# Kernel tuning notes

Hardware: AMD Instinct MI355X
Metric: run time of the kernel (lower is better)

Reference implementation:

```python
import jax, jax.numpy as jnp
import numpy as np

B, T, NIN, NMEM, NOUT = 8, 2048, 1024, 1024, 1024


def setup_inputs() -> dict:
    key = jax.random.key(0)
    ks = jax.random.split(key, 9)
    s_in = 1.0 / np.sqrt(NIN).astype(np.float32)
    s_mem = 1.0 / np.sqrt(NMEM).astype(np.float32)
    return {
        "x": jax.random.normal(ks[0], (B, T, NIN), jnp.float32),
        "mem": jnp.zeros((B, NMEM), jnp.float32),
        # torch Linear weights are [out_features, in_features]
        "wr_w": jax.random.normal(ks[1], (NMEM, NIN), jnp.float32) * s_in,
        "wr_b": jax.random.normal(ks[2], (NMEM,), jnp.float32) * s_in,
        "wi_w": jax.random.normal(ks[3], (NMEM, NIN), jnp.float32) * s_in,
        "wig_w": jax.random.normal(ks[4], (NMEM, NIN), jnp.float32) * s_in,
        "wig_b": jax.random.normal(ks[5], (NMEM,), jnp.float32) * s_in,
        "wog_w": jax.random.normal(ks[6], (NMEM, NIN), jnp.float32) * s_in,
        "wog_b": jax.random.normal(ks[7], (NMEM,), jnp.float32) * s_in,
        "wo_w": jax.random.normal(ks[8], (NOUT, NMEM), jnp.float32) * s_mem,
    }


def _sqrll_scan(xi, r, mem0):
    # linear recurrence: h_t = h_{t-1} * r_t + x_t, over time axis
    def step(h, inp):
        xt, rt = inp
        h = h * rt + xt
        return h, h

    # time-major for scan: [T, B, M]
    _, ys = jax.lax.scan(step, mem0, (jnp.swapaxes(xi, 0, 1), jnp.swapaxes(r, 0, 1)))
    return jnp.swapaxes(ys, 0, 1)  # [B, T, M]


def reference(x, mem, wr_w, wr_b, wi_w, wig_w, wig_b, wog_w, wog_b, wo_w):
    og = jax.nn.sigmoid(jnp.einsum("bti,mi->btm", x, wog_w) + wog_b)
    r = jax.nn.sigmoid(jnp.einsum("bti,mi->btm", x, wr_w) + wr_b)
    xi = jnp.einsum("bti,mi->btm", x, wi_w) * jax.nn.sigmoid(
        jnp.einsum("bti,mi->btm", x, wig_w) + wig_b
    )
    y = _sqrll_scan(xi, r, mem)  # [B, T, NMEM]
    mem_out = jax.lax.stop_gradient(y[:, -1])
    y = jax.nn.soft_sign(y) * og
    y = jnp.einsum("btm,om->bto", y, wo_w)
    return (y, mem_out)
```

## Files before the change

kernel.cpp:

```cpp
#include <hip/hip_runtime.h>
#include <hip/hip_bf16.h>
#include <cstdint>
#include <cstddef>

using bf16 = __hip_bfloat16;

typedef short s16x8 __attribute__((ext_vector_type(8)));
typedef short s16x4 __attribute__((ext_vector_type(4)));
typedef float f32x4 __attribute__((ext_vector_type(4)));

#define CH 32
#define CS 64

__device__ __align__(16) bf16  g_xb[16384 * 1024];
__device__ __align__(16) bf16  g_wb[5 * 1024 * 1024];
__device__ __align__(16) bf16  g_og[16384 * 1024];
__device__ float g_cA[CH * 8192];
__device__ float g_cB[CH * 8192];

__device__ inline short bfbits(float f) {
  unsigned x = __float_as_uint(f);
  return (short)((x + 0x7FFFu + ((x >> 16) & 1u)) >> 16);
}
__device__ inline float sigmoidf_(float z) { return 1.0f / (1.0f + __expf(-z)); }

__device__ inline void gload_lds16(const void* g, void* l) {
  __builtin_amdgcn_global_load_lds(
      (const __attribute__((address_space(1))) void*)g,
      (__attribute__((address_space(3))) void*)l, 16, 0, 0);
}

__global__ void conv_kernel(const float* __restrict__ src, bf16* __restrict__ dst, int n4) {
  int i = blockIdx.x * blockDim.x + threadIdx.x;
  const int stride = gridDim.x * blockDim.x;
  for (; i < n4; i += stride) {
    f32x4 v = ((const f32x4*)src)[i];
    s16x4 w;
    w[0] = bfbits(v[0]); w[1] = bfbits(v[1]);
    w[2] = bfbits(v[2]); w[3] = bfbits(v[3]);
    ((s16x4*)dst)[i] = w;
  }
}

__global__ __launch_bounds__(512, 2) void gemm_quad(
    const bf16* __restrict__ A,
    const bf16* __restrict__ B0, const bf16* __restrict__ B1,
    const bf16* __restrict__ B2, const bf16* __restrict__ B3,
    const float* __restrict__ bias_r, const float* __restrict__ bias_og,
    const float* __restrict__ bias_ig,
    float* __restrict__ Cr, bf16* __restrict__ Cog, bf16* __restrict__ Cxi,
    int M, int N, int K)
{
  __shared__ bf16 As[2][256 * 64];
  __shared__ bf16 Bs[2][4][64 * 64];

  const int tid  = threadIdx.x;
  const int wave = tid >> 6;
  const int lane = tid & 63;
  const int m0 = blockIdx.x * 256;
  const int n0 = blockIdx.y * 64;

  const int srow8 = lane >> 3;
  const int schk8 = ((lane & 7) ^ ((lane >> 3) & 7)) << 3;
  const bf16* Bm = (wave < 2) ? B0 : (wave < 4) ? B1 : (wave < 6) ? B2 : B3;
  const bf16* pAs = A  + (size_t)(m0 + wave * 32 + srow8) * K + schk8;
  const bf16* pBs = Bm + (size_t)(n0 + (wave & 1) * 32 + srow8) * K + schk8;

  const int lane15 = lane & 15;
  const int csel   = lane >> 4;
  int o[2];
  #pragma unroll
  for (int kk = 0; kk < 2; ++kk)
    o[kk] = lane15 * 64 + ((((kk << 2) + csel) ^ (lane15 & 7)) << 3);
  const int wmA = (wave & 3) * 4096;
  const int mlo = (wave >> 2) * 2;

  f32x4 accP[4][4] = {};
  f32x4 accQ[4][4] = {};

  auto stage = [&](int b, size_t koff) {
    #pragma unroll
    for (int q = 0; q < 4; ++q) {
      gload_lds16(pAs + (size_t)q * 8 * K + koff,
                  (void*)&As[b][wave * 2048 + q * 512]);
      gload_lds16(pBs + (size_t)q * 8 * K + koff,
                  (void*)&Bs[b][wave >> 1][(wave & 1) * 2048 + q * 512]);
    }
  };

  int buf = 0;
  stage(0, 0);
  asm volatile("s_waitcnt vmcnt(0)" ::: "memory");
  __builtin_amdgcn_s_barrier();
  __builtin_amdgcn_sched_barrier(0);

  for (int t = 0; t < 16; ++t) {
    if (t + 1 < 16) stage(buf ^ 1, (size_t)(t + 1) * 64);
    __builtin_amdgcn_sched_barrier(0);

    #pragma unroll
    for (int kk = 0; kk < 2; ++kk) {
      const bf16* aB  = &As[buf][wmA + o[kk]];
      const bf16* b0B = &Bs[buf][mlo][o[kk]];
      const bf16* b1B = &Bs[buf][mlo + 1][o[kk]];
      s16x8 af[4], f0[4], f1[4];
      #pragma unroll
      for (int i = 0; i < 4; ++i) af[i] = *(const s16x8*)(aB + i * 1024);
      #pragma unroll
      for (int j = 0; j < 4; ++j) {
        f0[j] = *(const s16x8*)(b0B + j * 1024);
        f1[j] = *(const s16x8*)(b1B + j * 1024);
      }
      __builtin_amdgcn_s_setprio(1);
      #pragma unroll
      for (int i = 0; i < 4; ++i)
        #pragma unroll
        for (int j = 0; j < 4; ++j) {
          accP[i][j] = __builtin_amdgcn_mfma_f32_16x16x32_bf16(af[i], f0[j], accP[i][j], 0, 0, 0);
          accQ[i][j] = __builtin_amdgcn_mfma_f32_16x16x32_bf16(af[i], f1[j], accQ[i][j], 0, 0, 0);
        }
      __builtin_amdgcn_s_setprio(0);
    }

    asm volatile("s_waitcnt vmcnt(0)" ::: "memory");
    __builtin_amdgcn_s_barrier();
    __builtin_amdgcn_sched_barrier(0);
    buf ^= 1;
  }

  const int rq = (lane >> 4) * 4;
  const int cl = lane & 15;
  const int wr0 = m0 + (wave & 3) * 64;
  if (wave < 4) {
    #pragma unroll
    for (int j = 0; j < 4; ++j) {
      const int gc = n0 + j * 16 + cl;
      const float bR = bias_r[gc];
      const float bO = bias_og[gc];
      #pragma unroll
      for (int i = 0; i < 4; ++i) {
        const int gr = wr0 + i * 16 + rq;
        #pragma unroll
        for (int rr = 0; rr < 4; ++rr) {
          const size_t idx = (size_t)(gr + rr) * N + gc;
          Cr[idx]  = sigmoidf_(accP[i][j][rr] + bR);
          Cog[idx] = __float2bfloat16(sigmoidf_(accQ[i][j][rr] + bO));
        }
      }
    }
  } else {
    #pragma unroll
    for (int j = 0; j < 4; ++j) {
      const int gc = n0 + j * 16 + cl;
      const float bG = bias_ig[gc];
      #pragma unroll
      for (int i = 0; i < 4; ++i) {
        const int gr = wr0 + i * 16 + rq;
        #pragma unroll
        for (int rr = 0; rr < 4; ++rr) {
          const size_t idx = (size_t)(gr + rr) * N + gc;
          Cxi[idx] = __float2bfloat16(accP[i][j][rr] * sigmoidf_(accQ[i][j][rr] + bG));
        }
      }
    }
  }
}

__global__ __launch_bounds__(512, 2) void gemm_single(
    const bf16* __restrict__ A, const bf16* __restrict__ Bw,
    float* __restrict__ C, int M, int N, int K)
{
  __shared__ bf16 As[3][256 * 64];
  __shared__ bf16 Bs[3][128 * 64];

  const int tid  = threadIdx.x;
  const int wave = tid >> 6;
  const int lane = tid & 63;
  const int m0 = blockIdx.x * 256;
  const int n0 = blockIdx.y * 128;
  const int wm = (wave >> 1) * 64;
  const int wn = (wave & 1) * 64;

  const int srow8 = lane >> 3;
  const int schk8 = ((lane & 7) ^ ((lane >> 3) & 7)) << 3;
  const bf16* pAs = A  + (size_t)(m0 + wave * 32 + srow8) * K + schk8;
  const bf16* pBs = Bw + (size_t)(n0 + wave * 16 + srow8) * K + schk8;

  const int lane15 = lane & 15;
  const int csel   = lane >> 4;
  int o[2];
  #pragma unroll
  for (int kk = 0; kk < 2; ++kk)
    o[kk] = lane15 * 64 + ((((kk << 2) + csel) ^ (lane15 & 7)) << 3);

  f32x4 acc[4][4] = {};

  auto stage = [&](int b, size_t koff) {
    #pragma unroll
    for (int q = 0; q < 4; ++q)
      gload_lds16(pAs + (size_t)q * 8 * K + koff,
                  (void*)&As[b][wave * 2048 + q * 512]);
    #pragma unroll
    for (int q = 0; q < 2; ++q)
      gload_lds16(pBs + (size_t)q * 8 * K + koff,
                  (void*)&Bs[b][wave * 1024 + q * 512]);
  };

  stage(0, 0);
  stage(1, 64);
  asm volatile("s_waitcnt vmcnt(6)" ::: "memory");
  __builtin_amdgcn_s_barrier();
  __builtin_amdgcn_sched_barrier(0);

  int cur = 0, nxt = 2;
  for (int t = 0; t < 16; ++t) {
    const bool pf = (t + 2 < 16);
    if (pf) stage(nxt, (size_t)(t + 2) * 64);
    __builtin_amdgcn_sched_barrier(0);

    #pragma unroll
    for (int kk = 0; kk < 2; ++kk) {
      const bf16* aB = &As[cur][wm * 64 + o[kk]];
      const bf16* bB = &Bs[cur][wn * 64 + o[kk]];
      s16x8 af[4], bfr[4];
      #pragma unroll
      for (int i = 0; i < 4; ++i) af[i] = *(const s16x8*)(aB + i * 1024);
      #pragma unroll
      for (int j = 0; j < 4; ++j) bfr[j] = *(const s16x8*)(bB + j * 1024);
      __builtin_amdgcn_s_setprio(1);
      #pragma unroll
      for (int i = 0; i < 4; ++i)
        #pragma unroll
        for (int j = 0; j < 4; ++j)
          acc[i][j] = __builtin_amdgcn_mfma_f32_16x16x32_bf16(af[i], bfr[j], acc[i][j], 0, 0, 0);
      __builtin_amdgcn_s_setprio(0);
    }

    if (pf) asm volatile("s_waitcnt vmcnt(6)" ::: "memory");
    else    asm volatile("s_waitcnt vmcnt(0)" ::: "memory");
    __builtin_amdgcn_s_barrier();
    __builtin_amdgcn_sched_barrier(0);

    cur = (cur + 1 == 3) ? 0 : cur + 1;
    nxt = (nxt + 1 == 3) ? 0 : nxt + 1;
  }

  const int rq = (lane >> 4) * 4;
  const int cl = lane & 15;
  #pragma unroll
  for (int j = 0; j < 4; ++j) {
    const int gc = n0 + wn + j * 16 + cl;
    #pragma unroll
    for (int i = 0; i < 4; ++i) {
      const int gr = m0 + wm + i * 16 + rq;
      #pragma unroll
      for (int rr = 0; rr < 4; ++rr)
        C[(size_t)(gr + rr) * N + gc] = acc[i][j][rr];
    }
  }
}

__global__ __launch_bounds__(256) void scan_p1(
    const float* __restrict__ r, const bf16* __restrict__ xi)
{
  const int bid = blockIdx.x;
  const int c   = bid >> 5;
  const int idx = (bid & 31) * 256 + threadIdx.x;
  const int b = idx >> 10, m = idx & 1023;
  const size_t base = ((size_t)b * 2048 + c * CS) * 1024 + m;
  float a = 1.0f, s = 0.0f;
  #pragma unroll 16
  for (int t = 0; t < CS; ++t) {
    const size_t o = base + (size_t)t * 1024;
    const float rv = r[o];
    const float xv = __bfloat162float(xi[o]);
    a *= rv;
    s = fmaf(s, rv, xv);
  }
  g_cA[c * 8192 + idx] = a;
  g_cB[c * 8192 + idx] = s;
}

__global__ __launch_bounds__(256) void scan_p2(
    const float* __restrict__ mem, float* __restrict__ memout)
{
  const int idx = blockIdx.x * 256 + threadIdx.x;
  float H = mem[idx];
  #pragma unroll
  for (int c = 0; c < CH; ++c) {
    const float a = g_cA[c * 8192 + idx];
    const float s = g_cB[c * 8192 + idx];
    g_cA[c * 8192 + idx] = H;
    H = fmaf(a, H, s);
  }
  memout[idx] = H;
}

__global__ __launch_bounds__(256) void scan_p3(
    const float* __restrict__ r, bf16* xi, const bf16* __restrict__ og)
{
  const int bid = blockIdx.x;
  const int c   = bid >> 5;
  const int idx = (bid & 31) * 256 + threadIdx.x;
  const int b = idx >> 10, m = idx & 1023;
  const size_t base = ((size_t)b * 2048 + c * CS) * 1024 + m;
  float h = g_cA[c * 8192 + idx];
  #pragma unroll 8
  for (int t = 0; t < CS; ++t) {
    const size_t o = base + (size_t)t * 1024;
    const float rv = r[o];
    const float xv = __bfloat162float(xi[o]);
    const float ov = __bfloat162float(og[o]);
    h = fmaf(h, rv, xv);
    xi[o] = __float2bfloat16(h / (1.0f + fabsf(h)) * ov);
  }
}

extern "C" void kernel_launch(void* const* d_in, const int* in_sizes, int n_in,
                              void* d_out, int out_size, void* d_ws, size_t ws_size,
                              hipStream_t stream)
{
  const float* x     = (const float*)d_in[0];
  const float* mem   = (const float*)d_in[1];
  const float* wr_w  = (const float*)d_in[2];
  const float* wr_b  = (const float*)d_in[3];
  const float* wi_w  = (const float*)d_in[4];
  const float* wig_w = (const float*)d_in[5];
  const float* wig_b = (const float*)d_in[6];
  const float* wog_w = (const float*)d_in[7];
  const float* wog_b = (const float*)d_in[8];
  const float* wo_w  = (const float*)d_in[9];
  float* out = (float*)d_out;

  const int M = 16384, N = 1024, K = 1024;
  const size_t MN = (size_t)M * N;

  float* r  = (float*)d_ws;
  bf16*  xi = (bf16*)((char*)d_ws + MN * 4);

  bf16* xb = nullptr, *wb = nullptr, *og = nullptr;
  hipGetSymbolAddress((void**)&xb, HIP_SYMBOL(g_xb));
  hipGetSymbolAddress((void**)&wb, HIP_SYMBOL(g_wb));
  hipGetSymbolAddress((void**)&og, HIP_SYMBOL(g_og));

  dim3 block(256);

  conv_kernel<<<dim3(2048), block, 0, stream>>>(x, xb, (int)(MN / 4));
  const int W4 = 1024 * 1024 / 4;
  conv_kernel<<<dim3(256), block, 0, stream>>>(wr_w,  wb + 0 * 1024 * 1024, W4);
  conv_kernel<<<dim3(256), block, 0, stream>>>(wi_w,  wb + 1 * 1024 * 1024, W4);
  conv_kernel<<<dim3(256), block, 0, stream>>>(wig_w, wb + 2 * 1024 * 1024, W4);
  conv_kernel<<<dim3(256), block, 0, stream>>>(wog_w, wb + 3 * 1024 * 1024, W4);
  conv_kernel<<<dim3(256), block, 0, stream>>>(wo_w,  wb + 4 * 1024 * 1024, W4);

  gemm_quad<<<dim3(64, 16), dim3(512), 0, stream>>>(
      xb,
      wb + 0 * 1024 * 1024,
      wb + 3 * 1024 * 1024,
      wb + 1 * 1024 * 1024,
      wb + 2 * 1024 * 1024,
      wr_b, wog_b, wig_b,
      r, og, xi, M, N, K);

  scan_p1<<<dim3(1024), block, 0, stream>>>(r, xi);
  scan_p2<<<dim3(32),   block, 0, stream>>>(mem, out + MN);
  scan_p3<<<dim3(1024), block, 0, stream>>>(r, xi, og);

  gemm_single<<<dim3(64, 8), dim3(512), 0, stream>>>(
      xi, wb + 4 * 1024 * 1024, out, M, N, K);
}
```

Measured before the change: 453.0 us.

## Deepen GEMM pipelines to 4-stage K=32 buffers and swap grid order

Both GEMM kernels now use K-tiles of 32 instead of 64 with a 4-deep LDS ring buffer. Three stages stay in flight, waited on with vmcnt counts instead of full drains. The grid is transposed so consecutive blocks share the same M rows and walk N, which should improve L2 reuse of the activation tiles. The cost is more barriers per K (32 iterations instead of 16) and fewer MFMAs between each sync.

```diff
diff --git a/kernel.cpp b/kernel.cpp
--- a/kernel.cpp
+++ b/kernel.cpp
@@ -51,82 +51,87 @@
     float* __restrict__ Cr, bf16* __restrict__ Cog, bf16* __restrict__ Cxi,
     int M, int N, int K)
 {
-  __shared__ bf16 As[2][256 * 64];
-  __shared__ bf16 Bs[2][4][64 * 64];
+  __shared__ bf16 As[4][256 * 32];
+  __shared__ bf16 Bs[4][4][64 * 32];
 
   const int tid  = threadIdx.x;
   const int wave = tid >> 6;
   const int lane = tid & 63;
-  const int m0 = blockIdx.x * 256;
-  const int n0 = blockIdx.y * 64;
-
-  const int srow8 = lane >> 3;
-  const int schk8 = ((lane & 7) ^ ((lane >> 3) & 7)) << 3;
+  const int n0 = blockIdx.x * 64;
+  const int m0 = blockIdx.y * 256;
+
+  const int srow16 = lane >> 2;
+  const int schk   = ((lane & 3) ^ ((lane >> 2) & 3)) << 3;
   const bf16* Bm = (wave < 2) ? B0 : (wave < 4) ? B1 : (wave < 6) ? B2 : B3;
-  const bf16* pAs = A  + (size_t)(m0 + wave * 32 + srow8) * K + schk8;
-  const bf16* pBs = Bm + (size_t)(n0 + (wave & 1) * 32 + srow8) * K + schk8;
+  const bf16* pAs = A  + (size_t)(m0 + wave * 32 + srow16) * K + schk;
+  const bf16* pBs = Bm + (size_t)(n0 + (wave & 1) * 32 + srow16) * K + schk;
+  const size_t krow16 = (size_t)16 * K;
 
   const int lane15 = lane & 15;
   const int csel   = lane >> 4;
-  int o[2];
-  #pragma unroll
-  for (int kk = 0; kk < 2; ++kk)
-    o[kk] = lane15 * 64 + ((((kk << 2) + csel) ^ (lane15 & 7)) << 3);
-  const int wmA = (wave & 3) * 4096;
+  const int o = lane15 * 32 + ((csel ^ (lane15 & 3)) << 3);
+  const int wmA = (wave & 3) * 2048;
   const int mlo = (wave >> 2) * 2;
 
   f32x4 accP[4][4] = {};
   f32x4 accQ[4][4] = {};
 
   auto stage = [&](int b, size_t koff) {
-    #pragma unroll
-    for (int q = 0; q < 4; ++q) {
-      gload_lds16(pAs + (size_t)q * 8 * K + koff,
-                  (void*)&As[b][wave * 2048 + q * 512]);
-      gload_lds16(pBs + (size_t)q * 8 * K + koff,
-                  (void*)&Bs[b][wave >> 1][(wave & 1) * 2048 + q * 512]);
+    bf16* as = &As[b][wave * 1024];
+    bf16* bs = &Bs[b][wave >> 1][(wave & 1) * 1024];
+    gload_lds16(pAs + koff,          (void*)as);
+    gload_lds16(pAs + krow16 + koff, (void*)(as + 512));
+    gload_lds16(pBs + koff,          (void*)bs);
+    gload_lds16(pBs + krow16 + koff, (void*)(bs + 512));
+  };
+
+  auto compute = [&](int c) {
+    const bf16* aB  = &As[c][wmA + o];
+    const bf16* b0B = &Bs[c][mlo][o];
+    const bf16* b1B = &Bs[c][mlo + 1][o];
+    s16x8 af[4], f0[4], f1[4];
+    #pragma unroll
+    for (int i = 0; i < 4; ++i) af[i] = *(const s16x8*)(aB + i * 512);
+    #pragma unroll
+    for (int j = 0; j < 4; ++j) {
+      f0[j] = *(const s16x8*)(b0B + j * 512);
+      f1[j] = *(const s16x8*)(b1B + j * 512);
     }
+    __builtin_amdgcn_s_setprio(1);
+    #pragma unroll
+    for (int i = 0; i < 4; ++i)
+      #pragma unroll
+      for (int j = 0; j < 4; ++j) {
+        accP[i][j] = __builtin_amdgcn_mfma_f32_16x16x32_bf16(af[i], f0[j], accP[i][j], 0, 0, 0);
+        accQ[i][j] = __builtin_amdgcn_mfma_f32_16x16x32_bf16(af[i], f1[j], accQ[i][j], 0, 0, 0);
+      }
+    __builtin_amdgcn_s_setprio(0);
   };
 
-  int buf = 0;
   stage(0, 0);
-  asm volatile("s_waitcnt vmcnt(0)" ::: "memory");
-  __builtin_amdgcn_s_barrier();
-  __builtin_amdgcn_sched_barrier(0);
-
-  for (int t = 0; t < 16; ++t) {
-    if (t + 1 < 16) stage(buf ^ 1, (size_t)(t + 1) * 64);
+  stage(1, 32);
+  stage(2, 64);
+  asm volatile("s_waitcnt vmcnt(8)" ::: "memory");
+  __builtin_amdgcn_s_barrier();
+  __builtin_amdgcn_sched_barrier(0);
+
+  for (int t = 0; t < 29; ++t) {
+    stage((t + 3) & 3, (size_t)(t + 3) * 32);
     __builtin_amdgcn_sched_barrier(0);
-
-    #pragma unroll
-    for (int kk = 0; kk < 2; ++kk) {
-      const bf16* aB  = &As[buf][wmA + o[kk]];
-      const bf16* b0B = &Bs[buf][mlo][o[kk]];
-      const bf16* b1B = &Bs[buf][mlo + 1][o[kk]];
-      s16x8 af[4], f0[4], f1[4];
-      #pragma unroll
-      for (int i = 0; i < 4; ++i) af[i] = *(const s16x8*)(aB + i * 1024);
-      #pragma unroll
-      for (int j = 0; j < 4; ++j) {
-        f0[j] = *(const s16x8*)(b0B + j * 1024);
-        f1[j] = *(const s16x8*)(b1B + j * 1024);
-      }
-      __builtin_amdgcn_s_setprio(1);
-      #pragma unroll
-      for (int i = 0; i < 4; ++i)
-        #pragma unroll
-        for (int j = 0; j < 4; ++j) {
-          accP[i][j] = __builtin_amdgcn_mfma_f32_16x16x32_bf16(af[i], f0[j], accP[i][j], 0, 0, 0);
-          accQ[i][j] = __builtin_amdgcn_mfma_f32_16x16x32_bf16(af[i], f1[j], accQ[i][j], 0, 0, 0);
-        }
-      __builtin_amdgcn_s_setprio(0);
-    }
-
-    asm volatile("s_waitcnt vmcnt(0)" ::: "memory");
+    compute(t & 3);
+    asm volatile("s_waitcnt vmcnt(8)" ::: "memory");
     __builtin_amdgcn_s_barrier();
     __builtin_amdgcn_sched_barrier(0);
-    buf ^= 1;
-  }
+  }
+  compute(29 & 3);
+  asm volatile("s_waitcnt vmcnt(4)" ::: "memory");
+  __builtin_amdgcn_s_barrier();
+  __builtin_amdgcn_sched_barrier(0);
+  compute(30 & 3);
+  asm volatile("s_waitcnt vmcnt(0)" ::: "memory");
+  __builtin_amdgcn_s_barrier();
+  __builtin_amdgcn_sched_barrier(0);
+  compute(31 & 3);
 
   const int rq = (lane >> 4) * 4;
   const int cl = lane & 15;
@@ -170,80 +175,77 @@
     const bf16* __restrict__ A, const bf16* __restrict__ Bw,
     float* __restrict__ C, int M, int N, int K)
 {
-  __shared__ bf16 As[3][256 * 64];
-  __shared__ bf16 Bs[3][128 * 64];
+  __shared__ bf16 As[4][256 * 32];
+  __shared__ bf16 Bs[4][128 * 32];
 
   const int tid  = threadIdx.x;
   const int wave = tid >> 6;
   const int lane = tid & 63;
-  const int m0 = blockIdx.x * 256;
-  const int n0 = blockIdx.y * 128;
+  const int n0 = blockIdx.x * 128;
+  const int m0 = blockIdx.y * 256;
   const int wm = (wave >> 1) * 64;
   const int wn = (wave & 1) * 64;
 
-  const int srow8 = lane >> 3;
-  const int schk8 = ((lane & 7) ^ ((lane >> 3) & 7)) << 3;
-  const bf16* pAs = A  + (size_t)(m0 + wave * 32 + srow8) * K + schk8;
-  const bf16* pBs = Bw + (size_t)(n0 + wave * 16 + srow8) * K + schk8;
+  const int srow16 = lane >> 2;
+  const int schk   = ((lane & 3) ^ ((lane >> 2) & 3)) << 3;
+  const bf16* pAs = A  + (size_t)(m0 + wave * 32 + srow16) * K + schk;
+  const bf16* pBs = Bw + (size_t)(n0 + wave * 16 + srow16) * K + schk;
+  const size_t krow16 = (size_t)16 * K;
 
   const int lane15 = lane & 15;
   const int csel   = lane >> 4;
-  int o[2];
-  #pragma unroll
-  for (int kk = 0; kk < 2; ++kk)
-    o[kk] = lane15 * 64 + ((((kk << 2) + csel) ^ (lane15 & 7)) << 3);
+  const int o = lane15 * 32 + ((csel ^ (lane15 & 3)) << 3);
 
   f32x4 acc[4][4] = {};
 
   auto stage = [&](int b, size_t koff) {
-    #pragma unroll
-    for (int q = 0; q < 4; ++q)
-      gload_lds16(pAs + (size_t)q * 8 * K + koff,
-                  (void*)&As[b][wave * 2048 + q * 512]);
-    #pragma unroll
-    for (int q = 0; q < 2; ++q)
-      gload_lds16(pBs + (size_t)q * 8 * K + koff,
-                  (void*)&Bs[b][wave * 1024 + q * 512]);
+    bf16* as = &As[b][wave * 1024];
+    gload_lds16(pAs + koff,          (void*)as);
+    gload_lds16(pAs + krow16 + koff, (void*)(as + 512));
+    gload_lds16(pBs + koff,          (void*)&Bs[b][wave * 512]);
   };
 
+  auto compute = [&](int c) {
+    const bf16* aB = &As[c][wm * 32 + o];
+    const bf16* bB = &Bs[c][wn * 32 + o];
+    s16x8 af[4], bfr[4];
+    #pragma unroll
+    for (int i = 0; i < 4; ++i) af[i] = *(const s16x8*)(aB + i * 512);
+    #pragma unroll
+    for (int j = 0; j < 4; ++j) bfr[j] = *(const s16x8*)(bB + j * 512);
+    __builtin_amdgcn_s_setprio(1);
+    #pragma unroll
+    for (int i = 0; i < 4; ++i)
+      #pragma unroll
+      for (int j = 0; j < 4; ++j)
+        acc[i][j] = __builtin_amdgcn_mfma_f32_16x16x32_bf16(af[i], bfr[j], acc[i][j], 0, 0, 0);
+    __builtin_amdgcn_s_setprio(0);
+  };
+
   stage(0, 0);
-  stage(1, 64);
+  stage(1, 32);
+  stage(2, 64);
   asm volatile("s_waitcnt vmcnt(6)" ::: "memory");
   __builtin_amdgcn_s_barrier();
   __builtin_amdgcn_sched_barrier(0);
 
-  int cur = 0, nxt = 2;
-  for (int t = 0; t < 16; ++t) {
-    const bool pf = (t + 2 < 16);
-    if (pf) stage(nxt, (size_t)(t + 2) * 64);
+  for (int t = 0; t < 29; ++t) {
+    stage((t + 3) & 3, (size_t)(t + 3) * 32);
     __builtin_amdgcn_sched_barrier(0);
-
-    #pragma unroll
-    for (int kk = 0; kk < 2; ++kk) {
-      const bf16* aB = &As[cur][wm * 64 + o[kk]];
-      const bf16* bB = &Bs[cur][wn * 64 + o[kk]];
-      s16x8 af[4], bfr[4];
-      #pragma unroll
-      for (int i = 0; i < 4; ++i) af[i] = *(const s16x8*)(aB + i * 1024);
-      #pragma unroll
-      for (int j = 0; j < 4; ++j) bfr[j] = *(const s16x8*)(bB + j * 1024);
-      __builtin_amdgcn_s_setprio(1);
-      #pragma unroll
-      for (int i = 0; i < 4; ++i)
-        #pragma unroll
-        for (int j = 0; j < 4; ++j)
-          acc[i][j] = __builtin_amdgcn_mfma_f32_16x16x32_bf16(af[i], bfr[j], acc[i][j], 0, 0, 0);
-      __builtin_amdgcn_s_setprio(0);
-    }
-
-    if (pf) asm volatile("s_waitcnt vmcnt(6)" ::: "memory");
-    else    asm volatile("s_waitcnt vmcnt(0)" ::: "memory");
+    compute(t & 3);
+    asm volatile("s_waitcnt vmcnt(6)" ::: "memory");
     __builtin_amdgcn_s_barrier();
     __builtin_amdgcn_sched_barrier(0);
-
-    cur = (cur + 1 == 3) ? 0 : cur + 1;
-    nxt = (nxt + 1 == 3) ? 0 : nxt + 1;
-  }
+  }
+  compute(29 & 3);
+  asm volatile("s_waitcnt vmcnt(3)" ::: "memory");
+  __builtin_amdgcn_s_barrier();
+  __builtin_amdgcn_sched_barrier(0);
+  compute(30 & 3);
+  asm volatile("s_waitcnt vmcnt(0)" ::: "memory");
+  __builtin_amdgcn_s_barrier();
+  __builtin_amdgcn_sched_barrier(0);
+  compute(31 & 3);
 
   const int rq = (lane >> 4) * 4;
   const int cl = lane & 15;
@@ -353,7 +355,7 @@
   conv_kernel<<<dim3(256), block, 0, stream>>>(wog_w, wb + 3 * 1024 * 1024, W4);
   conv_kernel<<<dim3(256), block, 0, stream>>>(wo_w,  wb + 4 * 1024 * 1024, W4);
 
-  gemm_quad<<<dim3(64, 16), dim3(512), 0, stream>>>(
+  gemm_quad<<<dim3(16, 64), dim3(512), 0, stream>>>(
       xb,
       wb + 0 * 1024 * 1024,
       wb + 3 * 1024 * 1024,
@@ -366,6 +368,6 @@
   scan_p2<<<dim3(32),   block, 0, stream>>>(mem, out + MN);
   scan_p3<<<dim3(1024), block, 0, stream>>>(r, xi, og);
 
-  gemm_single<<<dim3(64, 8), dim3(512), 0, stream>>>(
+  gemm_single<<<dim3(8, 64), dim3(512), 0, stream>>>(
       xi, wb + 4 * 1024 * 1024, out, M, N, K);
 }
```

New measurement: 509.8 us. +12.5%, slower.

## Load GEMM weight fragments directly into registers, bypassing LDS staging

Applied to the files above, without the earlier changes.

Both GEMM kernels stop staging the B (weight) tile through shared memory. Each wave now loads its MFMA B fragments straight from global memory into registers, double-buffered across k-steps, while A keeps a triple-buffered LDS pipeline. The warp tiling changes to 128 rows by 16 or 32 columns per wave, and the quad kernel now fuses all three epilogues in each wave. The aim is to cut LDS traffic and footprint and to overlap weight loads with compute, at the cost of uncoalesced global B loads and more register pressure.

```diff
diff --git a/kernel.cpp b/kernel.cpp
--- a/kernel.cpp
+++ b/kernel.cpp
@@ -51,117 +51,119 @@
     float* __restrict__ Cr, bf16* __restrict__ Cog, bf16* __restrict__ Cxi,
     int M, int N, int K)
 {
-  __shared__ bf16 As[2][256 * 64];
-  __shared__ bf16 Bs[2][4][64 * 64];
+  __shared__ bf16 As[3][256 * 64];
 
   const int tid  = threadIdx.x;
   const int wave = tid >> 6;
   const int lane = tid & 63;
   const int m0 = blockIdx.x * 256;
   const int n0 = blockIdx.y * 64;
+  const int mrow = wave >> 2;
+  const int ncol = wave & 3;
 
   const int srow8 = lane >> 3;
-  const int schk8 = ((lane & 7) ^ ((lane >> 3) & 7)) << 3;
-  const bf16* Bm = (wave < 2) ? B0 : (wave < 4) ? B1 : (wave < 6) ? B2 : B3;
-  const bf16* pAs = A  + (size_t)(m0 + wave * 32 + srow8) * K + schk8;
-  const bf16* pBs = Bm + (size_t)(n0 + (wave & 1) * 32 + srow8) * K + schk8;
+  const int schk  = ((lane & 7) ^ ((lane >> 3) & 7)) << 3;
+  const bf16* pAs = A + (size_t)(m0 + wave * 32 + srow8) * K + schk;
 
   const int lane15 = lane & 15;
   const int csel   = lane >> 4;
-  int o[2];
+  int oA[2];
   #pragma unroll
   for (int kk = 0; kk < 2; ++kk)
-    o[kk] = lane15 * 64 + ((((kk << 2) + csel) ^ (lane15 & 7)) << 3);
-  const int wmA = (wave & 3) * 4096;
-  const int mlo = (wave >> 2) * 2;
-
-  f32x4 accP[4][4] = {};
-  f32x4 accQ[4][4] = {};
-
-  auto stage = [&](int b, size_t koff) {
-    #pragma unroll
-    for (int q = 0; q < 4; ++q) {
-      gload_lds16(pAs + (size_t)q * 8 * K + koff,
-                  (void*)&As[b][wave * 2048 + q * 512]);
-      gload_lds16(pBs + (size_t)q * 8 * K + koff,
-                  (void*)&Bs[b][wave >> 1][(wave & 1) * 2048 + q * 512]);
-    }
-  };
-
-  int buf = 0;
-  stage(0, 0);
-  asm volatile("s_waitcnt vmcnt(0)" ::: "memory");
-  __builtin_amdgcn_s_barrier();
-  __builtin_amdgcn_sched_barrier(0);
-
-  for (int t = 0; t < 16; ++t) {
-    if (t + 1 < 16) stage(buf ^ 1, (size_t)(t + 1) * 64);
-    __builtin_amdgcn_sched_barrier(0);
-
+    oA[kk] = lane15 * 64 + ((((kk << 2) + csel) ^ (lane15 & 7)) << 3);
+
+  const size_t bOffL = (size_t)(n0 + ncol * 16 + lane15) * K + csel * 8;
+
+  f32x4 acc[4][8] = {};
+
+  auto stageA = [&](int b, int t) {
+    const size_t koff = (size_t)t * 64;
+    bf16* dst = &As[b][wave * 2048];
+    gload_lds16(pAs + koff,                   (void*)dst);
+    gload_lds16(pAs + koff + (size_t)8  * K,  (void*)(dst + 512));
+    gload_lds16(pAs + koff + (size_t)16 * K,  (void*)(dst + 1024));
+    gload_lds16(pAs + koff + (size_t)24 * K,  (void*)(dst + 1536));
+  };
+
+  auto loadB = [&](s16x8 (&d)[4][2], int t) {
+    const size_t kb = bOffL + (size_t)t * 64;
+    d[0][0] = *(const s16x8*)(B0 + kb); d[0][1] = *(const s16x8*)(B0 + kb + 32);
+    d[1][0] = *(const s16x8*)(B1 + kb); d[1][1] = *(const s16x8*)(B1 + kb + 32);
+    d[2][0] = *(const s16x8*)(B2 + kb); d[2][1] = *(const s16x8*)(B2 + kb + 32);
+    d[3][0] = *(const s16x8*)(B3 + kb); d[3][1] = *(const s16x8*)(B3 + kb + 32);
+  };
+
+  auto compute = [&](int t, const s16x8 (&bq)[4][2]) {
+    const bf16* Ab = &As[t % 3][mrow * 8192];
     #pragma unroll
     for (int kk = 0; kk < 2; ++kk) {
-      const bf16* aB  = &As[buf][wmA + o[kk]];
-      const bf16* b0B = &Bs[buf][mlo][o[kk]];
-      const bf16* b1B = &Bs[buf][mlo + 1][o[kk]];
-      s16x8 af[4], f0[4], f1[4];
-      #pragma unroll
-      for (int i = 0; i < 4; ++i) af[i] = *(const s16x8*)(aB + i * 1024);
-      #pragma unroll
-      for (int j = 0; j < 4; ++j) {
-        f0[j] = *(const s16x8*)(b0B + j * 1024);
-        f1[j] = *(const s16x8*)(b1B + j * 1024);
+      s16x8 af[8];
+      const int ob = oA[kk];
+      #pragma unroll
+      for (int i = 0; i < 8; ++i) af[i] = *(const s16x8*)(Ab + ob + i * 1024);
+      __builtin_amdgcn_s_setprio(1);
+      #pragma unroll
+      for (int i = 0; i < 8; ++i) {
+        acc[0][i] = __builtin_amdgcn_mfma_f32_16x16x32_bf16(af[i], bq[0][kk], acc[0][i], 0, 0, 0);
+        acc[1][i] = __builtin_amdgcn_mfma_f32_16x16x32_bf16(af[i], bq[1][kk], acc[1][i], 0, 0, 0);
+        acc[2][i] = __builtin_amdgcn_mfma_f32_16x16x32_bf16(af[i], bq[2][kk], acc[2][i], 0, 0, 0);
+        acc[3][i] = __builtin_amdgcn_mfma_f32_16x16x32_bf16(af[i], bq[3][kk], acc[3][i], 0, 0, 0);
       }
-      __builtin_amdgcn_s_setprio(1);
-      #pragma unroll
-      for (int i = 0; i < 4; ++i)
-        #pragma unroll
-        for (int j = 0; j < 4; ++j) {
-          accP[i][j] = __builtin_amdgcn_mfma_f32_16x16x32_bf16(af[i], f0[j], accP[i][j], 0, 0, 0);
-          accQ[i][j] = __builtin_amdgcn_mfma_f32_16x16x32_bf16(af[i], f1[j], accQ[i][j], 0, 0, 0);
-        }
       __builtin_amdgcn_s_setprio(0);
     }
-
-    asm volatile("s_waitcnt vmcnt(0)" ::: "memory");
+  };
+
+  s16x8 bEven[4][2], bOdd[4][2];
+
+  stageA(0, 0);
+  stageA(1, 1);
+  loadB(bEven, 0);
+  asm volatile("s_waitcnt vmcnt(12)" ::: "memory");
+  __builtin_amdgcn_s_barrier();
+  __builtin_amdgcn_sched_barrier(0);
+
+  #pragma unroll 1
+  for (int d = 0; d < 7; ++d) {
+    const int t = 2 * d;
+    stageA((t + 2) % 3, t + 2);
+    loadB(bOdd, t + 1);
+    __builtin_amdgcn_sched_barrier(0);
+    compute(t, bEven);
+    asm volatile("s_waitcnt vmcnt(12)" ::: "memory");
     __builtin_amdgcn_s_barrier();
     __builtin_amdgcn_sched_barrier(0);
-    buf ^= 1;
-  }
+
+    stageA((t + 3) % 3, t + 3);
+    loadB(bEven, t + 2);
+    __builtin_amdgcn_sched_barrier(0);
+    compute(t + 1, bOdd);
+    asm volatile("s_waitcnt vmcnt(12)" ::: "memory");
+    __builtin_amdgcn_s_barrier();
+    __builtin_amdgcn_sched_barrier(0);
+  }
+  loadB(bOdd, 15);
+  __builtin_amdgcn_sched_barrier(0);
+  compute(14, bEven);
+  asm volatile("s_waitcnt vmcnt(8)" ::: "memory");
+  __builtin_amdgcn_s_barrier();
+  __builtin_amdgcn_sched_barrier(0);
+  compute(15, bOdd);
 
   const int rq = (lane >> 4) * 4;
   const int cl = lane & 15;
-  const int wr0 = m0 + (wave & 3) * 64;
-  if (wave < 4) {
+  const int gc = n0 + ncol * 16 + cl;
+  const float bR = bias_r[gc];
+  const float bO = bias_og[gc];
+  const float bG = bias_ig[gc];
+  #pragma unroll
+  for (int i = 0; i < 8; ++i) {
+    const int gr = m0 + mrow * 128 + i * 16 + rq;
     #pragma unroll
-    for (int j = 0; j < 4; ++j) {
-      const int gc = n0 + j * 16 + cl;
-      const float bR = bias_r[gc];
-      const float bO = bias_og[gc];
-      #pragma unroll
-      for (int i = 0; i < 4; ++i) {
-        const int gr = wr0 + i * 16 + rq;
-        #pragma unroll
-        for (int rr = 0; rr < 4; ++rr) {
-          const size_t idx = (size_t)(gr + rr) * N + gc;
-          Cr[idx]  = sigmoidf_(accP[i][j][rr] + bR);
-          Cog[idx] = __float2bfloat16(sigmoidf_(accQ[i][j][rr] + bO));
-        }
-      }
-    }
-  } else {
-    #pragma unroll
-    for (int j = 0; j < 4; ++j) {
-      const int gc = n0 + j * 16 + cl;
-      const float bG = bias_ig[gc];
-      #pragma unroll
-      for (int i = 0; i < 4; ++i) {
-        const int gr = wr0 + i * 16 + rq;
-        #pragma unroll
-        for (int rr = 0; rr < 4; ++rr) {
-          const size_t idx = (size_t)(gr + rr) * N + gc;
-          Cxi[idx] = __float2bfloat16(accP[i][j][rr] * sigmoidf_(accQ[i][j][rr] + bG));
-        }
-      }
+    for (int rr = 0; rr < 4; ++rr) {
+      const size_t idx = (size_t)(gr + rr) * N + gc;
+      Cr[idx]  = sigmoidf_(acc[0][i][rr] + bR);
+      Cog[idx] = __float2bfloat16(sigmoidf_(acc[1][i][rr] + bO));
+      Cxi[idx] = __float2bfloat16(acc[2][i][rr] * sigmoidf_(acc[3][i][rr] + bG));
     }
   }
 }
@@ -171,91 +173,111 @@
     float* __restrict__ C, int M, int N, int K)
 {
   __shared__ bf16 As[3][256 * 64];
-  __shared__ bf16 Bs[3][128 * 64];
 
   const int tid  = threadIdx.x;
   const int wave = tid >> 6;
   const int lane = tid & 63;
   const int m0 = blockIdx.x * 256;
   const int n0 = blockIdx.y * 128;
-  const int wm = (wave >> 1) * 64;
-  const int wn = (wave & 1) * 64;
+  const int mrow = wave >> 2;
+  const int ncol = wave & 3;
 
   const int srow8 = lane >> 3;
-  const int schk8 = ((lane & 7) ^ ((lane >> 3) & 7)) << 3;
-  const bf16* pAs = A  + (size_t)(m0 + wave * 32 + srow8) * K + schk8;
-  const bf16* pBs = Bw + (size_t)(n0 + wave * 16 + srow8) * K + schk8;
+  const int schk  = ((lane & 7) ^ ((lane >> 3) & 7)) << 3;
+  const bf16* pAs = A + (size_t)(m0 + wave * 32 + srow8) * K + schk;
 
   const int lane15 = lane & 15;
   const int csel   = lane >> 4;
-  int o[2];
+  int oA[2];
   #pragma unroll
   for (int kk = 0; kk < 2; ++kk)
-    o[kk] = lane15 * 64 + ((((kk << 2) + csel) ^ (lane15 & 7)) << 3);
-
-  f32x4 acc[4][4] = {};
-
-  auto stage = [&](int b, size_t koff) {
-    #pragma unroll
-    for (int q = 0; q < 4; ++q)
-      gload_lds16(pAs + (size_t)q * 8 * K + koff,
-                  (void*)&As[b][wave * 2048 + q * 512]);
-    #pragma unroll
-    for (int q = 0; q < 2; ++q)
-      gload_lds16(pBs + (size_t)q * 8 * K + koff,
-                  (void*)&Bs[b][wave * 1024 + q * 512]);
-  };
-
-  stage(0, 0);
-  stage(1, 64);
-  asm volatile("s_waitcnt vmcnt(6)" ::: "memory");
-  __builtin_amdgcn_s_barrier();
-  __builtin_amdgcn_sched_barrier(0);
-
-  int cur = 0, nxt = 2;
-  for (int t = 0; t < 16; ++t) {
-    const bool pf = (t + 2 < 16);
-    if (pf) stage(nxt, (size_t)(t + 2) * 64);
-    __builtin_amdgcn_sched_barrier(0);
-
+    oA[kk] = lane15 * 64 + ((((kk << 2) + csel) ^ (lane15 & 7)) << 3);
+
+  const size_t bOff0 = (size_t)(n0 + ncol * 32 + lane15) * K + csel * 8;
+  const size_t bOff1 = bOff0 + (size_t)16 * K;
+
+  f32x4 acc[2][8] = {};
+
+  auto stageA = [&](int b, int t) {
+    const size_t koff = (size_t)t * 64;
+    bf16* dst = &As[b][wave * 2048];
+    gload_lds16(pAs + koff,                  (void*)dst);
+    gload_lds16(pAs + koff + (size_t)8  * K, (void*)(dst + 512));
+    gload_lds16(pAs + koff + (size_t)16 * K, (void*)(dst + 1024));
+    gload_lds16(pAs + koff + (size_t)24 * K, (void*)(dst + 1536));
+  };
+
+  auto loadB = [&](s16x8 (&d)[2][2], int t) {
+    const size_t kb = (size_t)t * 64;
+    d[0][0] = *(const s16x8*)(Bw + bOff0 + kb); d[0][1] = *(const s16x8*)(Bw + bOff0 + kb + 32);
+    d[1][0] = *(const s16x8*)(Bw + bOff1 + kb); d[1][1] = *(const s16x8*)(Bw + bOff1 + kb + 32);
+  };
+
+  auto compute = [&](int t, const s16x8 (&bq)[2][2]) {
+    const bf16* Ab = &As[t % 3][mrow * 8192];
     #pragma unroll
     for (int kk = 0; kk < 2; ++kk) {
-      const bf16* aB = &As[cur][wm * 64 + o[kk]];
-      const bf16* bB = &Bs[cur][wn * 64 + o[kk]];
-      s16x8 af[4], bfr[4];
-      #pragma unroll
-      for (int i = 0; i < 4; ++i) af[i] = *(const s16x8*)(aB + i * 1024);
-      #pragma unroll
-      for (int j = 0; j < 4; ++j) bfr[j] = *(const s16x8*)(bB + j * 1024);
+      s16x8 af[8];
+      const int ob = oA[kk];
+      #pragma unroll
+      for (int i = 0; i < 8; ++i) af[i] = *(const s16x8*)(Ab + ob + i * 1024);
       __builtin_amdgcn_s_setprio(1);
       #pragma unroll
-      for (int i = 0; i < 4; ++i)
-        #pragma unroll
-        for (int j = 0; j < 4; ++j)
-          acc[i][j] = __builtin_amdgcn_mfma_f32_16x16x32_bf16(af[i], bfr[j], acc[i][j], 0, 0, 0);
+      for (int i = 0; i < 8; ++i) {
+        acc[0][i] = __builtin_amdgcn_mfma_f32_16x16x32_bf16(af[i], bq[0][kk], acc[0][i], 0, 0, 0);
+        acc[1][i] = __builtin_amdgcn_mfma_f32_16x16x32_bf16(af[i], bq[1][kk], acc[1][i], 0, 0, 0);
+      }
       __builtin_amdgcn_s_setprio(0);
     }
-
-    if (pf) asm volatile("s_waitcnt vmcnt(6)" ::: "memory");
-    else    asm volatile("s_waitcnt vmcnt(0)" ::: "memory");
+  };
+
+  s16x8 bEven[2][2], bOdd[2][2];
+
+  stageA(0, 0);
+  stageA(1, 1);
+  loadB(bEven, 0);
+  asm volatile("s_waitcnt vmcnt(8)" ::: "memory");
+  __builtin_amdgcn_s_barrier();
+  __builtin_amdgcn_sched_barrier(0);
+
+  #pragma unroll 1
+  for (int d = 0; d < 7; ++d) {
+    const int t = 2 * d;
+    stageA((t + 2) % 3, t + 2);
+    loadB(bOdd, t + 1);
+    __builtin_amdgcn_sched_barrier(0);
+    compute(t, bEven);
+    asm volatile("s_waitcnt vmcnt(8)" ::: "memory");
     __builtin_amdgcn_s_barrier();
     __builtin_amdgcn_sched_barrier(0);
 
-    cur = (cur + 1 == 3) ? 0 : cur + 1;
-    nxt = (nxt + 1 == 3) ? 0 : nxt + 1;
-  }
+    stageA((t + 3) % 3, t + 3);
+    loadB(bEven, t + 2);
+    __builtin_amdgcn_sched_barrier(0);
+    compute(t + 1, bOdd);
+    asm volatile("s_waitcnt vmcnt(8)" ::: "memory");
+    __builtin_amdgcn_s_barrier();
+    __builtin_amdgcn_sched_barrier(0);
+  }
+  loadB(bOdd, 15);
+  __builtin_amdgcn_sched_barrier(0);
+  compute(14, bEven);
+  asm volatile("s_waitcnt vmcnt(4)" ::: "memory");
+  __builtin_amdgcn_s_barrier();
+  __builtin_amdgcn_sched_barrier(0);
+  compute(15, bOdd);
 
   const int rq = (lane >> 4) * 4;
   const int cl = lane & 15;
   #pragma unroll
-  for (int j = 0; j < 4; ++j) {
-    const int gc = n0 + wn + j * 16 + cl;
+  for (int j = 0; j < 2; ++j) {
+    const int gc = n0 + ncol * 32 + j * 16 + cl;
     #pragma unroll
-    for (int i = 0; i < 4; ++i) {
-      const int gr = m0 + wm + i * 16 + rq;
+    for (int i = 0; i < 8; ++i) {
+      const int gr = m0 + mrow * 128 + i * 16 + rq;
       #pragma unroll
       for (int rr = 0; rr < 4; ++rr)
-        C[(size_t)(gr + rr) * N + gc] = acc[i][j][rr];
+        C[(size_t)(gr + rr) * N + gc] = acc[j][i][rr];
     }
   }
 }
```

New measurement: 492.1 us. 8.6% more time.

## Shrink GEMM tiles to 128 rows, BK=32, triple-buffered 256-thread blocks

Applied to the files above, without the earlier changes.

Both GEMMs switch from 512-thread blocks with 256-row tiles and a 64-wide K step to 256-thread blocks with 128-row tiles and a 32-wide K step. Each uses a unified LDS buffer with a new 4-chunk XOR swizzle and a three-stage global_load_lds pipeline. The intent is more blocks for better CU fill and occupancy, plus deeper prefetch to hide load latency. In exchange, each block reuses less data, so more global and L2 traffic is needed, and there are twice as many barriers per K pass.

```diff
diff --git a/kernel.cpp b/kernel.cpp
--- a/kernel.cpp
+++ b/kernel.cpp
@@ -42,7 +42,7 @@
   }
 }
 
-__global__ __launch_bounds__(512, 2) void gemm_quad(
+__global__ __launch_bounds__(256, 2) void gemm_quad(
     const bf16* __restrict__ A,
     const bf16* __restrict__ B0, const bf16* __restrict__ B1,
     const bf16* __restrict__ B2, const bf16* __restrict__ B3,
@@ -51,87 +51,95 @@
     float* __restrict__ Cr, bf16* __restrict__ Cog, bf16* __restrict__ Cxi,
     int M, int N, int K)
 {
-  __shared__ bf16 As[2][256 * 64];
-  __shared__ bf16 Bs[2][4][64 * 64];
+  __shared__ bf16 Ls[3][12288];
 
   const int tid  = threadIdx.x;
   const int wave = tid >> 6;
   const int lane = tid & 63;
-  const int m0 = blockIdx.x * 256;
+  const int m0 = blockIdx.x * 128;
   const int n0 = blockIdx.y * 64;
-
-  const int srow8 = lane >> 3;
-  const int schk8 = ((lane & 7) ^ ((lane >> 3) & 7)) << 3;
-  const bf16* Bm = (wave < 2) ? B0 : (wave < 4) ? B1 : (wave < 6) ? B2 : B3;
-  const bf16* pAs = A  + (size_t)(m0 + wave * 32 + srow8) * K + schk8;
-  const bf16* pBs = Bm + (size_t)(n0 + (wave & 1) * 32 + srow8) * K + schk8;
+  const int pair = wave >> 1;
+  const int mh   = wave & 1;
+
+  const int lrow = lane >> 2;
+  const int schk = ((lane & 3) ^ ((lane >> 2) & 3) ^ ((lane >> 4) & 3)) << 3;
+  const bf16* ps[6];
+  int lofs[6];
+  #pragma unroll
+  for (int q = 0; q < 6; ++q) {
+    const int s = wave * 6 + q;
+    const bf16* base;
+    int rowbase;
+    if (s < 8) { base = A; rowbase = m0 + s * 16; }
+    else {
+      const int b = s - 8;
+      base = (b < 4) ? B0 : (b < 8) ? B1 : (b < 12) ? B2 : B3;
+      rowbase = n0 + (b & 3) * 16;
+    }
+    ps[q]   = base + (size_t)(rowbase + lrow) * K + schk;
+    lofs[q] = s * 512;
+  }
+
+  auto stage = [&](int b, int t) {
+    const size_t koff = (size_t)t * 32;
+    #pragma unroll
+    for (int q = 0; q < 6; ++q)
+      gload_lds16(ps[q] + koff, (void*)&Ls[b][lofs[q]]);
+  };
 
   const int lane15 = lane & 15;
   const int csel   = lane >> 4;
-  int o[2];
-  #pragma unroll
-  for (int kk = 0; kk < 2; ++kk)
-    o[kk] = lane15 * 64 + ((((kk << 2) + csel) ^ (lane15 & 7)) << 3);
-  const int wmA = (wave & 3) * 4096;
-  const int mlo = (wave >> 2) * 2;
+  const int swzc   = ((csel ^ (lane15 & 3) ^ ((lane15 >> 2) & 3)) << 3);
+  const int aBase  = (mh * 64 + lane15) * 32 + swzc;
+  const int bBaseP = 4096 + pair * 4096 + lane15 * 32 + swzc;
 
   f32x4 accP[4][4] = {};
   f32x4 accQ[4][4] = {};
 
-  auto stage = [&](int b, size_t koff) {
-    #pragma unroll
-    for (int q = 0; q < 4; ++q) {
-      gload_lds16(pAs + (size_t)q * 8 * K + koff,
-                  (void*)&As[b][wave * 2048 + q * 512]);
-      gload_lds16(pBs + (size_t)q * 8 * K + koff,
-                  (void*)&Bs[b][wave >> 1][(wave & 1) * 2048 + q * 512]);
-    }
+  auto compute = [&](int c) {
+    const bf16* Lb = &Ls[c][0];
+    s16x8 af[4], bP[4], bQ[4];
+    #pragma unroll
+    for (int i = 0; i < 4; ++i) af[i] = *(const s16x8*)(Lb + aBase + i * 512);
+    #pragma unroll
+    for (int j = 0; j < 4; ++j) {
+      bP[j] = *(const s16x8*)(Lb + bBaseP + j * 512);
+      bQ[j] = *(const s16x8*)(Lb + bBaseP + 2048 + j * 512);
+    }
+    __builtin_amdgcn_s_setprio(1);
+    #pragma unroll
+    for (int i = 0; i < 4; ++i)
+      #pragma unroll
+      for (int j = 0; j < 4; ++j) {
+        accP[i][j] = __builtin_amdgcn_mfma_f32_16x16x32_bf16(af[i], bP[j], accP[i][j], 0, 0, 0);
+        accQ[i][j] = __builtin_amdgcn_mfma_f32_16x16x32_bf16(af[i], bQ[j], accQ[i][j], 0, 0, 0);
+      }
+    __builtin_amdgcn_s_setprio(0);
   };
 
-  int buf = 0;
   stage(0, 0);
+  stage(1, 1);
+  asm volatile("s_waitcnt vmcnt(6)" ::: "memory");
+  __builtin_amdgcn_s_barrier();
+  __builtin_amdgcn_sched_barrier(0);
+
+  for (int t = 0; t < 30; ++t) {
+    stage((t + 2) % 3, t + 2);
+    __builtin_amdgcn_sched_barrier(0);
+    compute(t % 3);
+    asm volatile("s_waitcnt vmcnt(6)" ::: "memory");
+    __builtin_amdgcn_s_barrier();
+    __builtin_amdgcn_sched_barrier(0);
+  }
+  compute(0);
   asm volatile("s_waitcnt vmcnt(0)" ::: "memory");
   __builtin_amdgcn_s_barrier();
   __builtin_amdgcn_sched_barrier(0);
-
-  for (int t = 0; t < 16; ++t) {
-    if (t + 1 < 16) stage(buf ^ 1, (size_t)(t + 1) * 64);
-    __builtin_amdgcn_sched_barrier(0);
-
-    #pragma unroll
-    for (int kk = 0; kk < 2; ++kk) {
-      const bf16* aB  = &As[buf][wmA + o[kk]];
-      const bf16* b0B = &Bs[buf][mlo][o[kk]];
-      const bf16* b1B = &Bs[buf][mlo + 1][o[kk]];
-      s16x8 af[4], f0[4], f1[4];
-      #pragma unroll
-      for (int i = 0; i < 4; ++i) af[i] = *(const s16x8*)(aB + i * 1024);
-      #pragma unroll
-      for (int j = 0; j < 4; ++j) {
-        f0[j] = *(const s16x8*)(b0B + j * 1024);
-        f1[j] = *(const s16x8*)(b1B + j * 1024);
-      }
-      __builtin_amdgcn_s_setprio(1);
-      #pragma unroll
-      for (int i = 0; i < 4; ++i)
-        #pragma unroll
-        for (int j = 0; j < 4; ++j) {
-          accP[i][j] = __builtin_amdgcn_mfma_f32_16x16x32_bf16(af[i], f0[j], accP[i][j], 0, 0, 0);
-          accQ[i][j] = __builtin_amdgcn_mfma_f32_16x16x32_bf16(af[i], f1[j], accQ[i][j], 0, 0, 0);
-        }
-      __builtin_amdgcn_s_setprio(0);
-    }
-
-    asm volatile("s_waitcnt vmcnt(0)" ::: "memory");
-    __builtin_amdgcn_s_barrier();
-    __builtin_amdgcn_sched_barrier(0);
-    buf ^= 1;
-  }
+  compute(1);
 
   const int rq = (lane >> 4) * 4;
   const int cl = lane & 15;
-  const int wr0 = m0 + (wave & 3) * 64;
-  if (wave < 4) {
+  if (pair == 0) {
     #pragma unroll
     for (int j = 0; j < 4; ++j) {
       const int gc = n0 + j * 16 + cl;
@@ -139,7 +147,7 @@
       const float bO = bias_og[gc];
       #pragma unroll
       for (int i = 0; i < 4; ++i) {
-        const int gr = wr0 + i * 16 + rq;
+        const int gr = m0 + mh * 64 + i * 16 + rq;
         #pragma unroll
         for (int rr = 0; rr < 4; ++rr) {
           const size_t idx = (size_t)(gr + rr) * N + gc;
@@ -155,7 +163,7 @@
       const float bG = bias_ig[gc];
       #pragma unroll
       for (int i = 0; i < 4; ++i) {
-        const int gr = wr0 + i * 16 + rq;
+        const int gr = m0 + mh * 64 + i * 16 + rq;
         #pragma unroll
         for (int rr = 0; rr < 4; ++rr) {
           const size_t idx = (size_t)(gr + rr) * N + gc;
@@ -166,93 +174,90 @@
   }
 }
 
-__global__ __launch_bounds__(512, 2) void gemm_single(
+__global__ __launch_bounds__(256, 3) void gemm_single(
     const bf16* __restrict__ A, const bf16* __restrict__ Bw,
     float* __restrict__ C, int M, int N, int K)
 {
-  __shared__ bf16 As[3][256 * 64];
-  __shared__ bf16 Bs[3][128 * 64];
+  __shared__ bf16 Ls[3][8192];
 
   const int tid  = threadIdx.x;
   const int wave = tid >> 6;
   const int lane = tid & 63;
-  const int m0 = blockIdx.x * 256;
+  const int m0 = blockIdx.x * 128;
   const int n0 = blockIdx.y * 128;
-  const int wm = (wave >> 1) * 64;
-  const int wn = (wave & 1) * 64;
-
-  const int srow8 = lane >> 3;
-  const int schk8 = ((lane & 7) ^ ((lane >> 3) & 7)) << 3;
-  const bf16* pAs = A  + (size_t)(m0 + wave * 32 + srow8) * K + schk8;
-  const bf16* pBs = Bw + (size_t)(n0 + wave * 16 + srow8) * K + schk8;
+
+  const int lrow = lane >> 2;
+  const int schk = ((lane & 3) ^ ((lane >> 2) & 3) ^ ((lane >> 4) & 3)) << 3;
+  const bf16* ps[4];
+  int lofs[4];
+  #pragma unroll
+  for (int q = 0; q < 4; ++q) {
+    const int s = wave * 4 + q;
+    const bf16* base = (s < 8) ? A : Bw;
+    const int rowbase = (s < 8) ? (m0 + s * 16) : (n0 + (s - 8) * 16);
+    ps[q]   = base + (size_t)(rowbase + lrow) * K + schk;
+    lofs[q] = s * 512;
+  }
+
+  auto stage = [&](int b, int t) {
+    const size_t koff = (size_t)t * 32;
+    #pragma unroll
+    for (int q = 0; q < 4; ++q)
+      gload_lds16(ps[q] + koff, (void*)&Ls[b][lofs[q]]);
+  };
 
   const int lane15 = lane & 15;
   const int csel   = lane >> 4;
-  int o[2];
-  #pragma unroll
-  for (int kk = 0; kk < 2; ++kk)
-    o[kk] = lane15 * 64 + ((((kk << 2) + csel) ^ (lane15 & 7)) << 3);
-
-  f32x4 acc[4][4] = {};
-
-  auto stage = [&](int b, size_t koff) {
-    #pragma unroll
-    for (int q = 0; q < 4; ++q)
-      gload_lds16(pAs + (size_t)q * 8 * K + koff,
-                  (void*)&As[b][wave * 2048 + q * 512]);
-    #pragma unroll
-    for (int q = 0; q < 2; ++q)
-      gload_lds16(pBs + (size_t)q * 8 * K + koff,
-                  (void*)&Bs[b][wave * 1024 + q * 512]);
+  const int swzc   = ((csel ^ (lane15 & 3) ^ ((lane15 >> 2) & 3)) << 3);
+  const int aBase  = lane15 * 32 + swzc;
+  const int bBase  = 4096 + (wave * 32 + lane15) * 32 + swzc;
+
+  f32x4 acc[8][2] = {};
+
+  auto compute = [&](int c) {
+    const bf16* Lb = &Ls[c][0];
+    s16x8 af[8], bfr[2];
+    #pragma unroll
+    for (int i = 0; i < 8; ++i) af[i] = *(const s16x8*)(Lb + aBase + i * 512);
+    #pragma unroll
+    for (int j = 0; j < 2; ++j) bfr[j] = *(const s16x8*)(Lb + bBase + j * 512);
+    __builtin_amdgcn_s_setprio(1);
+    #pragma unroll
+    for (int i = 0; i < 8; ++i)
+      #pragma unroll
+      for (int j = 0; j < 2; ++j)
+        acc[i][j] = __builtin_amdgcn_mfma_f32_16x16x32_bf16(af[i], bfr[j], acc[i][j], 0, 0, 0);
+    __builtin_amdgcn_s_setprio(0);
   };
 
   stage(0, 0);
-  stage(1, 64);
-  asm volatile("s_waitcnt vmcnt(6)" ::: "memory");
+  stage(1, 1);
+  asm volatile("s_waitcnt vmcnt(4)" ::: "memory");
   __builtin_amdgcn_s_barrier();
   __builtin_amdgcn_sched_barrier(0);
 
-  int cur = 0, nxt = 2;
-  for (int t = 0; t < 16; ++t) {
-    const bool pf = (t + 2 < 16);
-    if (pf) stage(nxt, (size_t)(t + 2) * 64);
+  for (int t = 0; t < 30; ++t) {
+    stage((t + 2) % 3, t + 2);
     __builtin_amdgcn_sched_barrier(0);
-
-    #pragma unroll
-    for (int kk = 0; kk < 2; ++kk) {
-      const bf16* aB = &As[cur][wm * 64 + o[kk]];
-      const bf16* bB = &Bs[cur][wn * 64 + o[kk]];
-      s16x8 af[4], bfr[4];
-      #pragma unroll
-      for (int i = 0; i < 4; ++i) af[i] = *(const s16x8*)(aB + i * 1024);
-      #pragma unroll
-      for (int j = 0; j < 4; ++j) bfr[j] = *(const s16x8*)(bB + j * 1024);
-      __builtin_amdgcn_s_setprio(1);
-      #pragma unroll
-      for (int i = 0; i < 4; ++i)
-        #pragma unroll
-        for (int j = 0; j < 4; ++j)
-          acc[i][j] = __builtin_amdgcn_mfma_f32_16x16x32_bf16(af[i], bfr[j], acc[i][j], 0, 0, 0);
-      __builtin_amdgcn_s_setprio(0);
-    }
-
-    if (pf) asm volatile("s_waitcnt vmcnt(6)" ::: "memory");
-    else    asm volatile("s_waitcnt vmcnt(0)" ::: "memory");
+    compute(t % 3);
+    asm volatile("s_waitcnt vmcnt(4)" ::: "memory");
     __builtin_amdgcn_s_barrier();
     __builtin_amdgcn_sched_barrier(0);
-
-    cur = (cur + 1 == 3) ? 0 : cur + 1;
-    nxt = (nxt + 1 == 3) ? 0 : nxt + 1;
-  }
+  }
+  compute(0);
+  asm volatile("s_waitcnt vmcnt(0)" ::: "memory");
+  __builtin_amdgcn_s_barrier();
+  __builtin_amdgcn_sched_barrier(0);
+  compute(1);
 
   const int rq = (lane >> 4) * 4;
   const int cl = lane & 15;
   #pragma unroll
-  for (int j = 0; j < 4; ++j) {
-    const int gc = n0 + wn + j * 16 + cl;
-    #pragma unroll
-    for (int i = 0; i < 4; ++i) {
-      const int gr = m0 + wm + i * 16 + rq;
+  for (int j = 0; j < 2; ++j) {
+    const int gc = n0 + wave * 32 + j * 16 + cl;
+    #pragma unroll
+    for (int i = 0; i < 8; ++i) {
+      const int gr = m0 + i * 16 + rq;
       #pragma unroll
       for (int rr = 0; rr < 4; ++rr)
         C[(size_t)(gr + rr) * N + gc] = acc[i][j][rr];
@@ -353,7 +358,7 @@
   conv_kernel<<<dim3(256), block, 0, stream>>>(wog_w, wb + 3 * 1024 * 1024, W4);
   conv_kernel<<<dim3(256), block, 0, stream>>>(wo_w,  wb + 4 * 1024 * 1024, W4);
 
-  gemm_quad<<<dim3(64, 16), dim3(512), 0, stream>>>(
+  gemm_quad<<<dim3(128, 16), block, 0, stream>>>(
       xb,
       wb + 0 * 1024 * 1024,
       wb + 3 * 1024 * 1024,
@@ -366,6 +371,6 @@
   scan_p2<<<dim3(32),   block, 0, stream>>>(mem, out + MN);
   scan_p3<<<dim3(1024), block, 0, stream>>>(r, xi, og);
 
-  gemm_single<<<dim3(64, 8), dim3(512), 0, stream>>>(
+  gemm_single<<<dim3(128, 8), block, 0, stream>>>(
       xi, wb + 4 * 1024 * 1024, out, M, N, K);
 }
```

After: 455.9 us. About the same (+0.6%).
